# Optimization experiments

Measured on AMD Instinct MI355X. Metric: run time of the kernel, lower is better.

## Reference

```python
import jax, jax.numpy as jnp
import numpy as np

N, D, D_A, D_B, R = 512, 4096, 256, 256, 4
B = 2048
U_END = D_B * R            # 1024
V_END = U_END + R * D_A    # 2048
B_END = V_END + D_B        # 2304
LN_EPS = 1e-5


def setup_inputs() -> dict:
    key = jax.random.key(0)
    k1, k2, k3, k4 = jax.random.split(key, 4)
    return {
        "h_A": jax.random.normal(k1, (B, D_A), dtype=jnp.float32),
        "pool_vectors": jax.random.normal(k2, (N, D), dtype=jnp.float32) * 0.02,
        "alpha": jax.random.uniform(k3, (B, N), dtype=jnp.float32),
        "W_base": jax.random.normal(k4, (D_B, D_A), dtype=jnp.float32) * 0.01,
        "b_base": jnp.zeros((D_B,), dtype=jnp.float32),
        "gamma": jnp.array(0.01, dtype=jnp.float32),
        "ln_scale": jnp.ones((D_A,), dtype=jnp.float32),
        "ln_bias": jnp.zeros((D_A,), dtype=jnp.float32),
    }


def reference(h_A, pool_vectors, alpha, W_base, b_base, gamma, ln_scale, ln_bias):
    # --- assemble ---
    U = pool_vectors[:, :U_END].reshape(N, D_B, R)          # [N, d_B, r]
    V = pool_vectors[:, U_END:V_END].reshape(N, R, D_A)     # [N, r, d_A]
    bias = pool_vectors[:, V_END:B_END]                     # [N, d_B]
    UV = jnp.einsum('ndr,nre->nde', U, V)                   # [N, d_B, d_A]
    W_assembled = W_base[None] + jnp.einsum('bn,nde->bde', alpha, UV)  # [B, d_B, d_A]
    b_assembled = b_base[None] + jnp.einsum('bn,nd->bd', alpha, bias)  # [B, d_B]
    # --- apply + residual + LayerNorm ---
    h_t = jnp.einsum('ba,bca->bc', h_A, W_assembled) + b_assembled     # [B, d_B]
    y = h_A + gamma * h_t
    mu = jnp.mean(y, axis=-1, keepdims=True)
    var = jnp.var(y, axis=-1, keepdims=True)
    y_norm = (y - mu) * jax.lax.rsqrt(var + LN_EPS)
    return y_norm * ln_scale + ln_bias
```

## Files before the change

### kernel.cpp

```cpp
#include <hip/hip_runtime.h>
#include <hip/hip_bf16.h>


typedef __attribute__((ext_vector_type(8))) short bf16x8;
typedef __attribute__((ext_vector_type(4))) float f32x4;
typedef unsigned short ushort_t;

#define LDA_X 2816
#define N_POOL 512
#define D_POOL 4096

__device__ __forceinline__ void gld16(const ushort_t* g, ushort_t* l) {
    __builtin_amdgcn_global_load_lds((__attribute__((address_space(1))) void*)g,
                                     (__attribute__((address_space(3))) void*)l, 16, 0, 0);
}

__device__ __forceinline__ ushort_t bfb(float x) {
    union { __hip_bfloat16 h; ushort_t u; } c; c.h = __float2bfloat16(x); return c.u;
}

__device__ __forceinline__ float bf2f(ushort_t u) {
    union { unsigned int i; float f; } c; c.i = ((unsigned int)u) << 16; return c.f;
}

__device__ __forceinline__ void write4(ushort_t* p, float4 v) {
    ushort4 w = {bfb(v.x), bfb(v.y), bfb(v.z), bfb(v.w)};
    *(ushort4*)p = w;
}

__global__ __launch_bounds__(256) void kFront(const float* __restrict__ hA,
                                              const float* __restrict__ pool,
                                              const float* __restrict__ alpha,
                                              const float* __restrict__ Wb,
                                              ushort_t* __restrict__ Xu,
                                              ushort_t* __restrict__ Mt) {
    __shared__ __align__(16) ushort_t shmem[16384];
    ushort_t* As = shmem;
    ushort_t* Bs = shmem + 8192;
    const int t = threadIdx.x;
    const int bid = blockIdx.x;

    if (bid >= 1024) {
        const int b2 = bid - 1024;
        if (b2 < 512) {
            int idx = b2 * 256 + t, b = idx >> 6, a4 = (idx & 63) << 2;
            write4(Xu + (size_t)b * LDA_X + 2048 + a4, *(const float4*)&hA[(size_t)b * 256 + a4]);
        } else if (b2 < 1536) {
            int idx = (b2 - 512) * 256 + t, b = idx >> 7, j4 = (idx & 127) << 2;
            write4(Xu + (size_t)b * LDA_X + 2304 + j4, *(const float4*)&alpha[(size_t)b * 512 + j4]);
        } else if (b2 < 2048) {
            int idx = (b2 - 1536) * 256 + t, c = idx >> 9, n = idx & 511;
            write4(Mt + (size_t)c * LDA_X + (n << 2), *(const float4*)&pool[(size_t)n * D_POOL + (c << 2)]);
        } else if (b2 < 2112) {
            int idx = (b2 - 2048) * 256 + t, c = idx >> 6, q = (idx & 63) << 2;
            write4(Mt + (size_t)c * LDA_X + 2048 + q, *(const float4*)&Wb[(size_t)c * 256 + q]);
        } else {
            float* Lf = (float*)shmem;
            int tb = b2 - 2112;
            int j0 = (tb >> 2) * 64, c0t = (tb & 3) * 64;
            #pragma unroll
            for (int i = 0; i < 16; ++i) {
                int idx = i * 256 + t, jj = idx >> 6, cc = idx & 63;
                Lf[jj * 65 + cc] = pool[(size_t)(j0 + jj) * D_POOL + 2048 + c0t + cc];
            }
            __syncthreads();
            int cc = t >> 2, js = (t & 3) * 16;
            __align__(16) ushort_t u[16];
            #pragma unroll
            for (int j = 0; j < 16; ++j) u[j] = bfb(Lf[(js + j) * 65 + cc]);
            ushort_t* dst = Mt + (size_t)(c0t + cc) * LDA_X + 2304 + j0 + js;
            *(uint4*)dst = ((uint4*)u)[0];
            *(uint4*)(dst + 8) = ((uint4*)u)[1];
        }
        return;
    }

    const int w = t >> 6, l = t & 63, l16 = l & 15, l4 = l >> 4;
    const int wr = w >> 1, wc = w & 1;
    const int bm0 = (bid >> 5) * 64, bn0 = (bid & 31) * 64;
    const int row = t >> 2, cs = t & 3;

    f32x4 acc[2][2];
    #pragma unroll
    for (int i = 0; i < 2; ++i)
        #pragma unroll
        for (int j = 0; j < 2; ++j) acc[i][j] = (f32x4){0.f, 0.f, 0.f, 0.f};

    float4 aR[4], bR[4];
    const int kk = bn0 + row;
    const float* bbase = pool + (size_t)(kk >> 2) * D_POOL + 1024 + (kk & 3) * 256;
    const float* abase = hA + (size_t)(bm0 + row) * 256;

    auto loadRegs = [&](int step) {
        const int a0 = step * 64;
        #pragma unroll
        for (int p = 0; p < 4; ++p) {
            int c0 = (cs + p * 4) << 2;
            aR[p] = *(const float4*)(abase + a0 + c0);
            bR[p] = *(const float4*)(bbase + a0 + c0);
        }
    };
    auto writeLDS = [&](int buf) {
        #pragma unroll
        for (int p = 0; p < 4; ++p) {
            int c0 = (cs + p * 4) << 2;
            int off = row * 64 + (((c0 >> 3) ^ (row & 7)) << 3) + ((c0 >> 2) & 1) * 4;
            ushort4 ua = {bfb(aR[p].x), bfb(aR[p].y), bfb(aR[p].z), bfb(aR[p].w)};
            ushort4 ub = {bfb(bR[p].x), bfb(bR[p].y), bfb(bR[p].z), bfb(bR[p].w)};
            *(ushort4*)&As[buf * 4096 + off] = ua;
            *(ushort4*)&Bs[buf * 4096 + off] = ub;
        }
    };
    auto compute = [&](int buf) {
        bf16x8 af[2][2], bv[2][2];
        #pragma unroll
        for (int mi = 0; mi < 2; ++mi) {
            int arow = wr * 32 + mi * 16 + l16;
            #pragma unroll
            for (int ks = 0; ks < 2; ++ks)
                af[mi][ks] = *(const bf16x8*)&As[buf * 4096 + arow * 64 + (((ks * 4 + l4) ^ (arow & 7)) << 3)];
        }
        #pragma unroll
        for (int ni = 0; ni < 2; ++ni) {
            int brow = wc * 32 + ni * 16 + l16;
            #pragma unroll
            for (int ks = 0; ks < 2; ++ks)
                bv[ni][ks] = *(const bf16x8*)&Bs[buf * 4096 + brow * 64 + (((ks * 4 + l4) ^ (brow & 7)) << 3)];
        }
        #pragma unroll
        for (int ks = 0; ks < 2; ++ks)
            #pragma unroll
            for (int mi = 0; mi < 2; ++mi)
                #pragma unroll
                for (int ni = 0; ni < 2; ++ni)
                    acc[mi][ni] = __builtin_amdgcn_mfma_f32_16x16x32_bf16(af[mi][ks], bv[ni][ks], acc[mi][ni], 0, 0, 0);
    };

    loadRegs(0);
    writeLDS(0);
    __syncthreads();
    int cur = 0;
    #pragma unroll
    for (int it = 0; it < 3; ++it) {
        loadRegs(it + 1);
        compute(cur);
        writeLDS(cur ^ 1);
        __syncthreads();
        cur ^= 1;
    }
    compute(cur);

    __syncthreads();
    float* sc = (float*)shmem;
    #pragma unroll
    for (int mi = 0; mi < 2; ++mi)
        #pragma unroll
        for (int ni = 0; ni < 2; ++ni)
            #pragma unroll
            for (int e = 0; e < 4; ++e)
                sc[(wr * 32 + mi * 16 + l4 * 4 + e) * 64 + wc * 32 + ni * 16 + l16] = acc[mi][ni][e];
    __syncthreads();
    const int r2 = t >> 2, c0 = (t & 3) * 16;
    const float* arow = alpha + (size_t)(bm0 + r2) * N_POOL;
    __align__(16) ushort_t u[16];
    #pragma unroll
    for (int j = 0; j < 16; ++j)
        u[j] = bfb(sc[r2 * 64 + c0 + j] * arow[(bn0 + c0 + j) >> 2]);
    ushort_t* dst = Xu + (size_t)(bm0 + r2) * LDA_X + bn0 + c0;
    *(uint4*)dst = ((uint4*)u)[0];
    *(uint4*)(dst + 8) = ((uint4*)u)[1];
}

__global__ __launch_bounds__(256) void kB(const ushort_t* __restrict__ Xu,
                                          const ushort_t* __restrict__ Mt,
                                          ushort_t* __restrict__ part) {
    __shared__ __align__(16) ushort_t As[2][4096];
    __shared__ __align__(16) ushort_t Bs[2][4096];
    const int t = threadIdx.x;
    const int w = t >> 6, l = t & 63, l16 = l & 15, l4 = l >> 4;
    const int wr = w >> 1, wc = w & 1;
    const int bid = blockIdx.x;
    const int z = bid & 7;
    const int n = (bid >> 3) & 3;
    const int m = bid >> 5;
    const int bm0 = m * 64, bn0 = n * 64;
    const int steps = (z < 4) ? 6 : 5;
    const int kc0 = (z < 4) ? z * 384 : 1536 + (z - 4) * 320;
    const int srow = t >> 3;
    const int schunk = (t & 7) ^ (srow & 7);

    f32x4 acc[2][2];
    #pragma unroll
    for (int i = 0; i < 2; ++i)
        #pragma unroll
        for (int j = 0; j < 2; ++j) acc[i][j] = (f32x4){0.f, 0.f, 0.f, 0.f};

    auto stage = [&](int buf, int k0) {
        #pragma unroll
        for (int h = 0; h < 2; ++h) {
            gld16(Xu + (size_t)(bm0 + srow + h * 32) * LDA_X + k0 + schunk * 8,
                  &As[buf][h * 2048 + w * 512]);
            gld16(Mt + (size_t)(bn0 + srow + h * 32) * LDA_X + k0 + schunk * 8,
                  &Bs[buf][h * 2048 + w * 512]);
        }
    };
    auto compute = [&](int buf) {
        bf16x8 af[2][2], bv[2][2];
        #pragma unroll
        for (int mi = 0; mi < 2; ++mi) {
            int arow = wr * 32 + mi * 16 + l16;
            #pragma unroll
            for (int ks = 0; ks < 2; ++ks)
                af[mi][ks] = *(const bf16x8*)&As[buf][arow * 64 + (((ks * 4 + l4) ^ (arow & 7)) << 3)];
        }
        #pragma unroll
        for (int ni = 0; ni < 2; ++ni) {
            int brow = wc * 32 + ni * 16 + l16;
            #pragma unroll
            for (int ks = 0; ks < 2; ++ks)
                bv[ni][ks] = *(const bf16x8*)&Bs[buf][brow * 64 + (((ks * 4 + l4) ^ (brow & 7)) << 3)];
        }
        #pragma unroll
        for (int ks = 0; ks < 2; ++ks)
            #pragma unroll
            for (int mi = 0; mi < 2; ++mi)
                #pragma unroll
                for (int ni = 0; ni < 2; ++ni)
                    acc[mi][ni] = __builtin_amdgcn_mfma_f32_16x16x32_bf16(af[mi][ks], bv[ni][ks], acc[mi][ni], 0, 0, 0);
    };

    stage(0, kc0);
    __syncthreads();
    int cur = 0;
    for (int it = 0; it < steps - 1; ++it) {
        stage(cur ^ 1, kc0 + (it + 1) * 64);
        compute(cur);
        __syncthreads();
        cur ^= 1;
    }
    compute(cur);

    __syncthreads();
    float* sc = (float*)&As[0][0];
    #pragma unroll
    for (int mi = 0; mi < 2; ++mi)
        #pragma unroll
        for (int ni = 0; ni < 2; ++ni)
            #pragma unroll
            for (int e = 0; e < 4; ++e)
                sc[(wr * 32 + mi * 16 + l4 * 4 + e) * 64 + wc * 32 + ni * 16 + l16] = acc[mi][ni][e];
    __syncthreads();
    const int r2 = t >> 2, c0 = (t & 3) * 16;
    __align__(16) ushort_t u[16];
    #pragma unroll
    for (int j = 0; j < 16; ++j) u[j] = bfb(sc[r2 * 64 + c0 + j]);
    ushort_t* P = part + (size_t)z * (2048 * 256) + (size_t)(bm0 + r2) * 256 + bn0 + c0;
    *(uint4*)P = ((uint4*)u)[0];
    *(uint4*)(P + 8) = ((uint4*)u)[1];
}

__global__ __launch_bounds__(256) void kC(const ushort_t* __restrict__ part,
                                          const float* __restrict__ hA,
                                          const float* __restrict__ bb,
                                          const float* __restrict__ gamma_p,
                                          const float* __restrict__ lns,
                                          const float* __restrict__ lnb,
                                          float* __restrict__ out) {
    const int wave = threadIdx.x >> 6;
    const int lane = threadIdx.x & 63;
    const int b = blockIdx.x * 4 + wave;
    const float g = gamma_p[0];
    const size_t base = (size_t)b * 256 + lane * 4;

    float p0 = 0.f, p1 = 0.f, p2 = 0.f, p3 = 0.f;
    #pragma unroll
    for (int z = 0; z < 8; ++z) {
        ushort4 q = *(const ushort4*)&part[(size_t)z * 2048 * 256 + base];
        p0 += bf2f(q.x); p1 += bf2f(q.y); p2 += bf2f(q.z); p3 += bf2f(q.w);
    }
    float4 h  = *(const float4*)&hA[base];
    float4 b4 = *(const float4*)&bb[lane * 4];
    float y0 = h.x + g * (p0 + b4.x);
    float y1 = h.y + g * (p1 + b4.y);
    float y2 = h.z + g * (p2 + b4.z);
    float y3 = h.w + g * (p3 + b4.w);

    float sum = y0 + y1 + y2 + y3;
    float ss  = y0*y0 + y1*y1 + y2*y2 + y3*y3;
    #pragma unroll
    for (int off = 1; off < 64; off <<= 1) {
        sum += __shfl_xor(sum, off);
        ss  += __shfl_xor(ss, off);
    }
    float mu  = sum * (1.0f / 256.0f);
    float var = ss * (1.0f / 256.0f) - mu * mu;
    float inv = rsqrtf(var + 1e-5f);

    float4 sc = *(const float4*)&lns[lane * 4];
    float4 bi = *(const float4*)&lnb[lane * 4];
    float4 o;
    o.x = (y0 - mu) * inv * sc.x + bi.x;
    o.y = (y1 - mu) * inv * sc.y + bi.y;
    o.z = (y2 - mu) * inv * sc.z + bi.z;
    o.w = (y3 - mu) * inv * sc.w + bi.w;
    *(float4*)&out[base] = o;
}

extern "C" void kernel_launch(void* const* d_in, const int* in_sizes, int n_in,
                              void* d_out, int out_size, void* d_ws, size_t ws_size,
                              hipStream_t stream) {
    const float* hA    = (const float*)d_in[0];
    const float* pool  = (const float*)d_in[1];
    const float* alpha = (const float*)d_in[2];
    const float* Wb    = (const float*)d_in[3];
    const float* bb    = (const float*)d_in[4];
    const float* gamma = (const float*)d_in[5];
    const float* lns   = (const float*)d_in[6];
    const float* lnb   = (const float*)d_in[7];
    float* out = (float*)d_out;

    ushort_t* Xu   = (ushort_t*)d_ws;
    ushort_t* Mt   = Xu + (size_t)2048 * LDA_X;
    ushort_t* part = Mt + (size_t)256 * LDA_X;

    kFront<<<3168, 256, 0, stream>>>(hA, pool, alpha, Wb, Xu, Mt);
    kB<<<1024, 256, 0, stream>>>(Xu, Mt, part);
    kC<<<512, 256, 0, stream>>>(part, hA, bb, gamma, lns, lnb, out);
}
```

Baseline: 30.38 us.

## Compute base-weight and bias GEMMs in front kernel, shrink kB K-range

The front kernel no longer copies h_A, alpha, W_base and the transposed bias slice into the concatenated K-extended operands. It instead computes h_A·W_base^T and alpha·bias directly as two extra GEMM block groups, writing them as partial slices 8 and 9. kB now covers only the 2048-wide UV part with a fixed 4-step loop per split, and kC sums ten partials. This removes the bf16 staging copies and the uneven K-splits in kB, at the cost of more partial traffic in kC and a strided bias load with scalar LDS transposes.

```diff
diff --git a/kernel.cpp b/kernel.cpp
--- a/kernel.cpp
+++ b/kernel.cpp
@@ -33,51 +33,22 @@
                                               const float* __restrict__ alpha,
                                               const float* __restrict__ Wb,
                                               ushort_t* __restrict__ Xu,
-                                              ushort_t* __restrict__ Mt) {
+                                              ushort_t* __restrict__ Mt,
+                                              ushort_t* __restrict__ part) {
     __shared__ __align__(16) ushort_t shmem[16384];
     ushort_t* As = shmem;
     ushort_t* Bs = shmem + 8192;
     const int t = threadIdx.x;
     const int bid = blockIdx.x;
 
-    if (bid >= 1024) {
-        const int b2 = bid - 1024;
-        if (b2 < 512) {
-            int idx = b2 * 256 + t, b = idx >> 6, a4 = (idx & 63) << 2;
-            write4(Xu + (size_t)b * LDA_X + 2048 + a4, *(const float4*)&hA[(size_t)b * 256 + a4]);
-        } else if (b2 < 1536) {
-            int idx = (b2 - 512) * 256 + t, b = idx >> 7, j4 = (idx & 127) << 2;
-            write4(Xu + (size_t)b * LDA_X + 2304 + j4, *(const float4*)&alpha[(size_t)b * 512 + j4]);
-        } else if (b2 < 2048) {
-            int idx = (b2 - 1536) * 256 + t, c = idx >> 9, n = idx & 511;
-            write4(Mt + (size_t)c * LDA_X + (n << 2), *(const float4*)&pool[(size_t)n * D_POOL + (c << 2)]);
-        } else if (b2 < 2112) {
-            int idx = (b2 - 2048) * 256 + t, c = idx >> 6, q = (idx & 63) << 2;
-            write4(Mt + (size_t)c * LDA_X + 2048 + q, *(const float4*)&Wb[(size_t)c * 256 + q]);
-        } else {
-            float* Lf = (float*)shmem;
-            int tb = b2 - 2112;
-            int j0 = (tb >> 2) * 64, c0t = (tb & 3) * 64;
-            #pragma unroll
-            for (int i = 0; i < 16; ++i) {
-                int idx = i * 256 + t, jj = idx >> 6, cc = idx & 63;
-                Lf[jj * 65 + cc] = pool[(size_t)(j0 + jj) * D_POOL + 2048 + c0t + cc];
-            }
-            __syncthreads();
-            int cc = t >> 2, js = (t & 3) * 16;
-            __align__(16) ushort_t u[16];
-            #pragma unroll
-            for (int j = 0; j < 16; ++j) u[j] = bfb(Lf[(js + j) * 65 + cc]);
-            ushort_t* dst = Mt + (size_t)(c0t + cc) * LDA_X + 2304 + j0 + js;
-            *(uint4*)dst = ((uint4*)u)[0];
-            *(uint4*)(dst + 8) = ((uint4*)u)[1];
-        }
+    if (bid >= 1024 && bid < 1536) {
+        int idx = (bid - 1024) * 256 + t, c = idx >> 9, n = idx & 511;
+        write4(Mt + (size_t)c * LDA_X + (n << 2), *(const float4*)&pool[(size_t)n * D_POOL + (c << 2)]);
         return;
     }
 
     const int w = t >> 6, l = t & 63, l16 = l & 15, l4 = l >> 4;
     const int wr = w >> 1, wc = w & 1;
-    const int bm0 = (bid >> 5) * 64, bn0 = (bid & 31) * 64;
     const int row = t >> 2, cs = t & 3;
 
     f32x4 acc[2][2];
@@ -87,20 +58,8 @@
         for (int j = 0; j < 2; ++j) acc[i][j] = (f32x4){0.f, 0.f, 0.f, 0.f};
 
     float4 aR[4], bR[4];
-    const int kk = bn0 + row;
-    const float* bbase = pool + (size_t)(kk >> 2) * D_POOL + 1024 + (kk & 3) * 256;
-    const float* abase = hA + (size_t)(bm0 + row) * 256;
-
-    auto loadRegs = [&](int step) {
-        const int a0 = step * 64;
-        #pragma unroll
-        for (int p = 0; p < 4; ++p) {
-            int c0 = (cs + p * 4) << 2;
-            aR[p] = *(const float4*)(abase + a0 + c0);
-            bR[p] = *(const float4*)(bbase + a0 + c0);
-        }
-    };
-    auto writeLDS = [&](int buf) {
+
+    auto writeLDS_AB = [&](int buf) {
         #pragma unroll
         for (int p = 0; p < 4; ++p) {
             int c0 = (cs + p * 4) << 2;
@@ -135,40 +94,148 @@
                 for (int ni = 0; ni < 2; ++ni)
                     acc[mi][ni] = __builtin_amdgcn_mfma_f32_16x16x32_bf16(af[mi][ks], bv[ni][ks], acc[mi][ni], 0, 0, 0);
     };
-
-    loadRegs(0);
-    writeLDS(0);
-    __syncthreads();
-    int cur = 0;
-    #pragma unroll
-    for (int it = 0; it < 3; ++it) {
-        loadRegs(it + 1);
+    auto epilogueLDS = [&]() {
+        __syncthreads();
+        float* sc = (float*)shmem;
+        #pragma unroll
+        for (int mi = 0; mi < 2; ++mi)
+            #pragma unroll
+            for (int ni = 0; ni < 2; ++ni)
+                #pragma unroll
+                for (int e = 0; e < 4; ++e)
+                    sc[(wr * 32 + mi * 16 + l4 * 4 + e) * 64 + wc * 32 + ni * 16 + l16] = acc[mi][ni][e];
+        __syncthreads();
+    };
+
+    if (bid < 1024) {
+        const int bm0 = (bid >> 5) * 64, bn0 = (bid & 31) * 64;
+        const int kk = bn0 + row;
+        const float* bbase = pool + (size_t)(kk >> 2) * D_POOL + 1024 + (kk & 3) * 256;
+        const float* abase = hA + (size_t)(bm0 + row) * 256;
+        auto loadRegs = [&](int step) {
+            const int a0 = step * 64;
+            #pragma unroll
+            for (int p = 0; p < 4; ++p) {
+                int c0 = (cs + p * 4) << 2;
+                aR[p] = *(const float4*)(abase + a0 + c0);
+                bR[p] = *(const float4*)(bbase + a0 + c0);
+            }
+        };
+        loadRegs(0); writeLDS_AB(0); __syncthreads();
+        int cur = 0;
+        #pragma unroll
+        for (int it = 0; it < 3; ++it) {
+            loadRegs(it + 1);
+            compute(cur);
+            writeLDS_AB(cur ^ 1);
+            __syncthreads();
+            cur ^= 1;
+        }
         compute(cur);
-        writeLDS(cur ^ 1);
-        __syncthreads();
-        cur ^= 1;
-    }
-    compute(cur);
-
-    __syncthreads();
-    float* sc = (float*)shmem;
-    #pragma unroll
-    for (int mi = 0; mi < 2; ++mi)
-        #pragma unroll
-        for (int ni = 0; ni < 2; ++ni)
-            #pragma unroll
-            for (int e = 0; e < 4; ++e)
-                sc[(wr * 32 + mi * 16 + l4 * 4 + e) * 64 + wc * 32 + ni * 16 + l16] = acc[mi][ni][e];
-    __syncthreads();
-    const int r2 = t >> 2, c0 = (t & 3) * 16;
-    const float* arow = alpha + (size_t)(bm0 + r2) * N_POOL;
-    __align__(16) ushort_t u[16];
-    #pragma unroll
-    for (int j = 0; j < 16; ++j)
-        u[j] = bfb(sc[r2 * 64 + c0 + j] * arow[(bn0 + c0 + j) >> 2]);
-    ushort_t* dst = Xu + (size_t)(bm0 + r2) * LDA_X + bn0 + c0;
-    *(uint4*)dst = ((uint4*)u)[0];
-    *(uint4*)(dst + 8) = ((uint4*)u)[1];
+        epilogueLDS();
+        float* sc = (float*)shmem;
+        const int r2 = t >> 2, c0 = (t & 3) * 16;
+        const float* arow = alpha + (size_t)(bm0 + r2) * N_POOL;
+        __align__(16) ushort_t u[16];
+        #pragma unroll
+        for (int j = 0; j < 16; ++j)
+            u[j] = bfb(sc[r2 * 64 + c0 + j] * arow[(bn0 + c0 + j) >> 2]);
+        ushort_t* dst = Xu + (size_t)(bm0 + r2) * LDA_X + bn0 + c0;
+        *(uint4*)dst = ((uint4*)u)[0];
+        *(uint4*)(dst + 8) = ((uint4*)u)[1];
+        return;
+    }
+
+    if (bid < 1664) {
+        const int b2 = bid - 1536;
+        const int bm0 = (b2 >> 2) * 64, bc0 = (b2 & 3) * 64;
+        const float* abase = hA + (size_t)(bm0 + row) * 256;
+        const float* bbase = Wb + (size_t)(bc0 + row) * 256;
+        auto loadRegs = [&](int step) {
+            const int a0 = step * 64;
+            #pragma unroll
+            for (int p = 0; p < 4; ++p) {
+                int c0 = (cs + p * 4) << 2;
+                aR[p] = *(const float4*)(abase + a0 + c0);
+                bR[p] = *(const float4*)(bbase + a0 + c0);
+            }
+        };
+        loadRegs(0); writeLDS_AB(0); __syncthreads();
+        int cur = 0;
+        #pragma unroll
+        for (int it = 0; it < 3; ++it) {
+            loadRegs(it + 1);
+            compute(cur);
+            writeLDS_AB(cur ^ 1);
+            __syncthreads();
+            cur ^= 1;
+        }
+        compute(cur);
+        epilogueLDS();
+        float* sc = (float*)shmem;
+        const int r2 = t >> 2, c0 = (t & 3) * 16;
+        __align__(16) ushort_t u[16];
+        #pragma unroll
+        for (int j = 0; j < 16; ++j) u[j] = bfb(sc[r2 * 64 + c0 + j]);
+        ushort_t* P = part + (size_t)8 * (2048 * 256) + (size_t)(bm0 + r2) * 256 + bc0 + c0;
+        *(uint4*)P = ((uint4*)u)[0];
+        *(uint4*)(P + 8) = ((uint4*)u)[1];
+        return;
+    }
+
+    {
+        const int b2 = bid - 1664;
+        const int bm0 = (b2 >> 2) * 64, bc0 = (b2 & 3) * 64;
+        const float* abase = alpha + (size_t)(bm0 + row) * N_POOL;
+        const int cg = t & 63;
+        const int jg = t >> 6;
+        float bRv[16];
+        auto loadRegsB = [&](int step) {
+            const int j0 = step * 64;
+            #pragma unroll
+            for (int p = 0; p < 4; ++p) {
+                int c0 = (cs + p * 4) << 2;
+                aR[p] = *(const float4*)(abase + j0 + c0);
+            }
+            #pragma unroll
+            for (int p = 0; p < 16; ++p)
+                bRv[p] = pool[(size_t)(j0 + jg * 16 + p) * D_POOL + 2048 + bc0 + cg];
+        };
+        auto writeLDSB = [&](int buf) {
+            #pragma unroll
+            for (int p = 0; p < 4; ++p) {
+                int c0 = (cs + p * 4) << 2;
+                int off = row * 64 + (((c0 >> 3) ^ (row & 7)) << 3) + ((c0 >> 2) & 1) * 4;
+                ushort4 ua = {bfb(aR[p].x), bfb(aR[p].y), bfb(aR[p].z), bfb(aR[p].w)};
+                *(ushort4*)&As[buf * 4096 + off] = ua;
+            }
+            #pragma unroll
+            for (int p = 0; p < 16; ++p) {
+                int jj = jg * 16 + p;
+                Bs[buf * 4096 + cg * 64 + (((jj >> 3) ^ (cg & 7)) << 3) + (jj & 7)] = bfb(bRv[p]);
+            }
+        };
+        loadRegsB(0); writeLDSB(0); __syncthreads();
+        int cur = 0;
+        #pragma unroll
+        for (int it = 0; it < 7; ++it) {
+            loadRegsB(it + 1);
+            compute(cur);
+            writeLDSB(cur ^ 1);
+            __syncthreads();
+            cur ^= 1;
+        }
+        compute(cur);
+        epilogueLDS();
+        float* sc = (float*)shmem;
+        const int r2 = t >> 2, c0 = (t & 3) * 16;
+        __align__(16) ushort_t u[16];
+        #pragma unroll
+        for (int j = 0; j < 16; ++j) u[j] = bfb(sc[r2 * 64 + c0 + j]);
+        ushort_t* P = part + (size_t)9 * (2048 * 256) + (size_t)(bm0 + r2) * 256 + bc0 + c0;
+        *(uint4*)P = ((uint4*)u)[0];
+        *(uint4*)(P + 8) = ((uint4*)u)[1];
+    }
 }
 
 __global__ __launch_bounds__(256) void kB(const ushort_t* __restrict__ Xu,
@@ -184,8 +251,7 @@
     const int n = (bid >> 3) & 3;
     const int m = bid >> 5;
     const int bm0 = m * 64, bn0 = n * 64;
-    const int steps = (z < 4) ? 6 : 5;
-    const int kc0 = (z < 4) ? z * 384 : 1536 + (z - 4) * 320;
+    const int kc0 = z * 256;
     const int srow = t >> 3;
     const int schunk = (t & 7) ^ (srow & 7);
 
@@ -232,7 +298,8 @@
     stage(0, kc0);
     __syncthreads();
     int cur = 0;
-    for (int it = 0; it < steps - 1; ++it) {
+    #pragma unroll
+    for (int it = 0; it < 3; ++it) {
         stage(cur ^ 1, kc0 + (it + 1) * 64);
         compute(cur);
         __syncthreads();
@@ -274,7 +341,7 @@
 
     float p0 = 0.f, p1 = 0.f, p2 = 0.f, p3 = 0.f;
     #pragma unroll
-    for (int z = 0; z < 8; ++z) {
+    for (int z = 0; z < 10; ++z) {
         ushort4 q = *(const ushort4*)&part[(size_t)z * 2048 * 256 + base];
         p0 += bf2f(q.x); p1 += bf2f(q.y); p2 += bf2f(q.z); p3 += bf2f(q.w);
     }
@@ -323,7 +390,7 @@
     ushort_t* Mt   = Xu + (size_t)2048 * LDA_X;
     ushort_t* part = Mt + (size_t)256 * LDA_X;
 
-    kFront<<<3168, 256, 0, stream>>>(hA, pool, alpha, Wb, Xu, Mt);
+    kFront<<<1792, 256, 0, stream>>>(hA, pool, alpha, Wb, Xu, Mt, part);
     kB<<<1024, 256, 0, stream>>>(Xu, Mt, part);
     kC<<<512, 256, 0, stream>>>(part, hA, bb, gamma, lns, lnb, out);
 }
```

Result: slower. 35.39 us (+16.5%).
